# Kernel optimization log

Measured on AMD Instinct MI355X. Metric: run time of the kernel, lower is better.

The kernel has to match this reference:

```python
import jax, jax.numpy as jnp
import numpy as np

NODES_PER_GRAPH = 1430  # hard-coded stride in the original forward
GENE0 = 1421            # first gene node index per graph
N_HEADS = 9


def gcn_conv(x, W, b, src, dst, n):
    """PyG-style GCNConv: D^-1/2 (A+I) D^-1/2 X W + b (self-loops added)."""
    h = x @ W  # [N, out]
    ones = jnp.ones(src.shape, jnp.float32)
    deg = jax.ops.segment_sum(ones, dst, num_segments=n) + 1.0  # +1 self-loop
    dinv = jax.lax.rsqrt(deg)
    norm = dinv[src] * dinv[dst]  # [E]
    agg = jax.ops.segment_sum(norm[:, None] * h[src], dst, num_segments=n)
    agg = agg + (dinv * dinv)[:, None] * h  # self-loop contribution
    return agg + b


def setup_inputs() -> dict:
    key = jax.random.key(0)
    ks = jax.random.split(key, 8)
    n_graphs = 512
    n = NODES_PER_GRAPH * n_graphs  # 732160 nodes
    e = n * 8                        # avg degree 8
    x = jax.random.normal(ks[0], (n, 1), jnp.float32)
    edge_index = jax.random.randint(ks[1], (2, e), 0, n, jnp.int32)
    y = jnp.zeros((n_graphs * N_HEADS,), jnp.int32)  # only y.size(0) is used
    W1 = jax.random.normal(ks[2], (1, 16), jnp.float32) * 0.5
    b1 = jnp.zeros((16,), jnp.float32)
    W2 = jax.random.normal(ks[3], (16, 16), jnp.float32) * 0.25
    b2 = jnp.zeros((16,), jnp.float32)
    fw1 = jax.random.normal(ks[4], (N_HEADS, 16, 8), jnp.float32) * 0.25
    fb1 = jnp.zeros((N_HEADS, 8), jnp.float32)
    fw2 = jax.random.normal(ks[5], (N_HEADS, 8, 1), jnp.float32) * 0.35
    fb2 = jnp.zeros((N_HEADS, 1), jnp.float32)
    return {"x": x, "edge_index": edge_index, "y": y, "W1": W1, "b1": b1,
            "W2": W2, "b2": b2, "fw1": fw1, "fb1": fb1, "fw2": fw2, "fb2": fb2}


def reference(x, edge_index, y, W1, b1, W2, b2, fw1, fb1, fw2, fb2):
    n = x.shape[0]
    src, dst = edge_index[0], edge_index[1]
    h = jax.nn.relu(gcn_conv(x, W1, b1, src, dst, n))
    # F.dropout(p=0.4) treated as identity (deterministic eval reference)
    h = jax.nn.relu(gcn_conv(h, W2, b2, src, dst, n))
    n_graphs = y.shape[0] // N_HEADS
    # fused version of the per-gene gather loop: idx[g, k] = 1421+g + k*1430
    idx = (GENE0 + jnp.arange(N_HEADS)[:, None]
           + jnp.arange(n_graphs)[None, :] * NODES_PER_GRAPH)  # [9, G]
    g = h[idx]  # [9, G, 16]
    z = jax.nn.relu(jnp.einsum('gnf,gfh->gnh', g, fw1) + fb1[:, None, :])
    pred = jnp.einsum('gnh,gho->gno', z, fw2) + fb2[:, None, :]  # [9, G, 1]
    return tuple(pred[i] for i in range(N_HEADS))
```

## Files before the change

### kernel.cpp

```cpp
#include <hip/hip_runtime.h>

#define NODES 1430
#define GENE0 1421
#define NHEADS 9
#define HBINS 131072
#define HWORDS (HBINS / 8)
#define BHIST 1024
#define GMAX 64
#define QCAP 1024

__device__ __forceinline__ float frelu(float v) { return v > 0.f ? v : 0.f; }

__global__ __launch_bounds__(BHIST, 4)
void k_hist(const int* __restrict__ esrc, const int* __restrict__ edst,
            unsigned int* __restrict__ copies,
            int* __restrict__ gene_cnt, int* __restrict__ gene_src,
            unsigned int* __restrict__ flagw,
            int e, int K, int R) {
    __shared__ unsigned int lds[HWORDS];
    int id = blockIdx.x;
    int k, r;
    if ((K & 7) == 0) {
        int xcd = id & 7;
        int slot = id >> 3;
        int cin = slot / R;
        k = xcd * (K >> 3) + cin;
        r = slot - cin * R;
    } else {
        k = id / R;
        r = id - k * R;
    }
    const int tid = threadIdx.x;
    {
        uint4* l4 = (uint4*)lds;
        for (int w = tid; w < HWORDS / 4; w += BHIST) l4[w] = make_uint4(0, 0, 0, 0);
    }
    __syncthreads();

    const unsigned int lo = (unsigned int)r * HBINS;
    const int e4 = e >> 2;
    const int Q = (e4 + K - 1) / K;
    const int beg = k * Q;
    const int end = min(beg + Q, e4);
    const int4* ed4 = (const int4*)edst;
    const int len = (end > beg) ? (end - beg) : 0;
    const int eighth = len >> 3;

    auto proc = [&](int4 d4) {
#pragma unroll
        for (int c = 0; c < 4; c++) {
            unsigned int d = (unsigned int)((&d4.x)[c]);
            unsigned int rel = d - lo;
            if (rel < HBINS)
                atomicAdd(&lds[rel >> 3], 1u << ((rel & 7u) * 4u));
        }
    };

    for (int i = tid; i < eighth; i += BHIST) {
        int j0 = beg + i;
        int4 v0 = ed4[j0];
        int4 v1 = ed4[j0 + eighth];
        int4 v2 = ed4[j0 + 2 * eighth];
        int4 v3 = ed4[j0 + 3 * eighth];
        int4 v4 = ed4[j0 + 4 * eighth];
        int4 v5 = ed4[j0 + 5 * eighth];
        int4 v6 = ed4[j0 + 6 * eighth];
        int4 v7 = ed4[j0 + 7 * eighth];
        proc(v0); proc(v1); proc(v2); proc(v3);
        proc(v4); proc(v5); proc(v6); proc(v7);
    }
    for (int i = (eighth << 3) + tid; i < len; i += BHIST) {
        proc(ed4[beg + i]);
    }

    {
        int sbeg = beg + (int)(((long long)len * r) / R);
        int send = beg + (int)(((long long)len * (r + 1)) / R);
        for (int j = sbeg + tid; j < send; j += BHIST) {
            int4 d4 = ed4[j];
#pragma unroll
            for (int c = 0; c < 4; c++) {
                unsigned int d = (unsigned int)((&d4.x)[c]);
                unsigned int graph = d / NODES;
                unsigned int pos = d - graph * NODES;
                if (pos >= GENE0) {
                    int s = esrc[4 * j + c];
                    atomicOr(&flagw[(unsigned)s >> 5], 1u << (s & 31));
                    int g = (int)(graph * NHEADS + (pos - GENE0));
                    int p = atomicAdd(gene_cnt + g, 1);
                    if (p < GMAX) gene_src[(g << 6) + p] = s;
                }
            }
        }
    }

    if (k == 0) {
        for (int j = (e4 << 2) + tid; j < e; j += BHIST) {
            unsigned int d = (unsigned int)edst[j];
            unsigned int rel = d - lo;
            if (rel < HBINS)
                atomicAdd(&lds[rel >> 3], 1u << ((rel & 7u) * 4u));
            if (r == 0) {
                unsigned int graph = d / NODES;
                unsigned int pos = d - graph * NODES;
                if (pos >= GENE0) {
                    int s = esrc[j];
                    atomicOr(&flagw[(unsigned)s >> 5], 1u << (s & 31));
                    int g = (int)(graph * NHEADS + (pos - GENE0));
                    int p = atomicAdd(gene_cnt + g, 1);
                    if (p < GMAX) gene_src[(g << 6) + p] = s;
                }
            }
        }
    }
    __syncthreads();
    uint4* dst4 = (uint4*)(copies + ((size_t)k * R + r) * HWORDS);
    const uint4* l4 = (const uint4*)lds;
    for (int w = tid; w < HWORDS / 4; w += BHIST) dst4[w] = l4[w];
}

__global__ void k_reduce(const unsigned int* __restrict__ copies,
                         const float* __restrict__ x,
                         float2* __restrict__ dx, float* __restrict__ t,
                         unsigned int* __restrict__ flagw,
                         int n, int K, int Wtot) {
    int w = blockIdx.x * blockDim.x + threadIdx.x;
    if (w >= Wtot) return;
    const unsigned int M = 0x0F0F0F0Fu;
    unsigned int ev[8] = {0, 0, 0, 0, 0, 0, 0, 0};
    unsigned int od[8] = {0, 0, 0, 0, 0, 0, 0, 0};
    int k = 0;
    for (; k + 8 <= K; k += 8) {
#pragma unroll
        for (int s = 0; s < 8; s++) {
            unsigned int u = copies[(size_t)(k + s) * Wtot + w];
            ev[s] += u & M; od[s] += (u >> 4) & M;
        }
    }
    for (; k < K; k++) {
        unsigned int u = copies[(size_t)k * Wtot + w];
        ev[0] += u & M; od[0] += (u >> 4) & M;
    }
    unsigned int evn = ((ev[0] + ev[1]) + (ev[2] + ev[3])) + ((ev[4] + ev[5]) + (ev[6] + ev[7]));
    unsigned int odd = ((od[0] + od[1]) + (od[2] + od[3])) + ((od[4] + od[5]) + (od[6] + od[7]));
    int i0 = w << 3;
    float v[8];
#pragma unroll
    for (int b = 0; b < 4; b++) {
        v[2 * b]     = (float)((evn >> (8 * b)) & 0xFFu);
        v[2 * b + 1] = (float)((odd >> (8 * b)) & 0xFFu);
    }
#pragma unroll
    for (int b = 0; b < 8; b++) v[b] = rsqrtf(v[b] + 1.f);
    float4 z4 = {0.f, 0.f, 0.f, 0.f};
    if (i0 + 7 < n) {
        float4 xa = *(const float4*)(x + i0);
        float4 xb = *(const float4*)(x + i0 + 4);
        float4 p0 = {v[0], v[0] * xa.x, v[1], v[1] * xa.y};
        float4 p1 = {v[2], v[2] * xa.z, v[3], v[3] * xa.w};
        float4 p2 = {v[4], v[4] * xb.x, v[5], v[5] * xb.y};
        float4 p3 = {v[6], v[6] * xb.z, v[7], v[7] * xb.w};
        float4* dst = (float4*)(dx + i0);
        dst[0] = p0; dst[1] = p1; dst[2] = p2; dst[3] = p3;
        *(float4*)(t + i0) = z4;
        *(float4*)(t + i0 + 4) = z4;
    } else {
        for (int b = 0; b < 8; b++)
            if (i0 + b < n) {
                float xv = x[i0 + b];
                dx[i0 + b] = make_float2(v[b], v[b] * xv);
                t[i0 + b] = 0.f;
            }
    }
#pragma unroll
    for (int b = 0; b < 8; b++) {
        int i = i0 + b;
        if (i < n) {
            unsigned int graph = (unsigned int)i / NODES;
            unsigned int pos = (unsigned int)i - graph * NODES;
            if (pos >= GENE0) atomicOr(&flagw[(unsigned)i >> 5], 1u << (i & 31));
        }
    }
}

__global__ __launch_bounds__(256, 8)
void k_l1_scatter(const int* __restrict__ esrc, const int* __restrict__ edst,
                  const float2* __restrict__ dx,
                  const unsigned int* __restrict__ flagw,
                  float* __restrict__ t, int e) {
    __shared__ int2 q[QCAP];
    __shared__ int qn;
    const int tid = threadIdx.x;
    if (tid == 0) qn = 0;
    __syncthreads();

    const int4* ed4 = (const int4*)edst;
    const int4* es4 = (const int4*)esrc;
    const int e4 = e >> 2;
    const int g0 = blockIdx.x * 512;
#pragma unroll
    for (int u = 0; u < 2; u++) {
        int gi = g0 + u * 256 + tid;
        if (gi < e4) {
            int4 dd = ed4[gi];
            int4 ss = es4[gi];
#pragma unroll
            for (int c = 0; c < 4; c++) {
                int d = (&dd.x)[c];
                if ((flagw[(unsigned)d >> 5] >> (d & 31)) & 1u) {
                    int p = atomicAdd(&qn, 1);
                    if (p < QCAP) q[p] = make_int2((&ss.x)[c], d);
                    else atomicAdd(t + d, dx[(&ss.x)[c]].y);
                }
            }
        }
    }
    if (blockIdx.x == 0) {
        for (int j = (e4 << 2) + tid; j < e; j += 256) {
            int d = edst[j];
            if ((flagw[(unsigned)d >> 5] >> (d & 31)) & 1u) {
                int s = esrc[j];
                atomicAdd(t + d, dx[s].y);
            }
        }
    }
    __syncthreads();
    int m = min(qn, QCAP);
    for (int i = tid; i < m; i += 256) {
        int2 sd = q[i];
        atomicAdd(t + sd.y, dx[sd.x].y);
    }
}

__global__ void k_gene_final(const int* __restrict__ gene_cnt, const int* __restrict__ gene_src,
                             const float* __restrict__ t, const float2* __restrict__ dx,
                             const float* __restrict__ W1, const float* __restrict__ b1,
                             const float* __restrict__ W2, const float* __restrict__ b2,
                             const float* __restrict__ fw1, const float* __restrict__ fb1,
                             const float* __restrict__ fw2, const float* __restrict__ fb2,
                             float* __restrict__ out, int NG, int G) {
    int wid = (blockIdx.x * blockDim.x + threadIdx.x) >> 6;
    int lane = threadIdx.x & 63;
    if (wid >= NG) return;
    int g = wid;
    int graph = g / NHEADS;
    int head = g - graph * NHEADS;
    int node = graph * NODES + GENE0 + head;
    const int c = lane & 15;
    const int slot = lane >> 4;

    int cnt = min(gene_cnt[g], GMAX);

    float w1r[16], b1r[16], w2c[16];
#pragma unroll
    for (int kk = 0; kk < 16; kk++) {
        w1r[kk] = W1[kk];
        b1r[kk] = b1[kk];
        w2c[kk] = W2[kk * 16 + c];
    }
    float2 dn2 = dx[node];
    float tn = t[node];

    float acc = 0.f;
    const int base = g << 6;
    for (int i = slot; i < cnt; i += 8) {
        int s0 = gene_src[base + i];
        int i1 = i + 4;
        int s1 = (i1 < cnt) ? gene_src[base + i1] : -1;
        float2 a2 = dx[s0];
        float ta = t[s0];
        float2 b2v = (s1 >= 0) ? dx[s1] : make_float2(0.f, 0.f);
        float tb = (s1 >= 0) ? t[s1] : 0.f;
        {
            float us = a2.x * ta + a2.x * a2.y;
            float m = 0.f;
#pragma unroll
            for (int kk = 0; kk < 16; kk++)
                m += frelu(us * w1r[kk] + b1r[kk]) * w2c[kk];
            acc += a2.x * m;
        }
        if (s1 >= 0) {
            float us = b2v.x * tb + b2v.x * b2v.y;
            float m = 0.f;
#pragma unroll
            for (int kk = 0; kk < 16; kk++)
                m += frelu(us * w1r[kk] + b1r[kk]) * w2c[kk];
            acc += b2v.x * m;
        }
    }
    acc += __shfl_xor(acc, 16, 64);
    acc += __shfl_xor(acc, 32, 64);

    float dn = dn2.x;
    float un = dn * tn + dn * dn2.y;
    float h2 = 0.f;
#pragma unroll
    for (int kk = 0; kk < 16; kk++)
        h2 += frelu(un * w1r[kk] + b1r[kk]) * w2c[kk];
    float h = frelu(dn * acc + dn * dn * h2 + b2[c]);

    float hv[16];
#pragma unroll
    for (int c2 = 0; c2 < 16; c2++) hv[c2] = __shfl(h, c2, 64);

    int kk = lane & 7;
    float z = fb1[head * 8 + kk];
#pragma unroll
    for (int c2 = 0; c2 < 16; c2++) z += hv[c2] * fw1[head * 128 + c2 * 8 + kk];
    float term = frelu(z) * fw2[head * 8 + kk];
    term += __shfl_xor(term, 1, 64);
    term += __shfl_xor(term, 2, 64);
    term += __shfl_xor(term, 4, 64);
    if (lane == 0) out[head * G + graph] = fb2[head] + term;
}

extern "C" void kernel_launch(void* const* d_in, const int* in_sizes, int n_in,
                              void* d_out, int out_size, void* d_ws, size_t ws_size,
                              hipStream_t stream) {
    const float* x   = (const float*)d_in[0];
    const int*   ei  = (const int*)d_in[1];
    const float* W1  = (const float*)d_in[3];
    const float* b1  = (const float*)d_in[4];
    const float* W2  = (const float*)d_in[5];
    const float* b2  = (const float*)d_in[6];
    const float* fw1 = (const float*)d_in[7];
    const float* fb1 = (const float*)d_in[8];
    const float* fw2 = (const float*)d_in[9];
    const float* fb2 = (const float*)d_in[10];

    int n = in_sizes[0];
    int e = in_sizes[1] / 2;
    int G = in_sizes[2] / NHEADS;
    int NG = G * NHEADS;
    const int* esrc = ei;
    const int* edst = ei + e;

    char* ws = (char*)d_ws;
    size_t off = 0;
    auto alloc = [&](size_t bytes) {
        char* p = ws + off;
        off += (bytes + 255) & ~(size_t)255;
        return p;
    };
    int*   gene_cnt      = (int*)alloc((size_t)NG * 4);
    unsigned int* flagw  = (unsigned int*)alloc((size_t)((n + 31) / 32) * 4);
    size_t zero_bytes    = off;
    int*    gene_src     = (int*)alloc((size_t)NG * GMAX * 4);
    float*  t            = (float*)alloc((size_t)n * 4);
    float2* dx           = (float2*)alloc((size_t)n * 8);
    size_t fixed         = off;

    int R = (n + HBINS - 1) / HBINS;
    size_t per_copy = (size_t)R * HWORDS * 4;
    int K = 80;
    if (fixed + (size_t)K * per_copy > ws_size) {
        size_t avail = (ws_size > fixed) ? (ws_size - fixed) : 0;
        int kfit = (int)(avail / per_copy);
        if (kfit >= 8) kfit &= ~7;
        K = kfit < 1 ? 1 : (kfit < K ? kfit : K);
    }
    unsigned int* copies = (unsigned int*)alloc((size_t)K * per_copy);
    (void)n_in; (void)out_size;

    hipMemsetAsync(d_ws, 0, zero_bytes, stream);

    const int B = 256;
    k_hist<<<K * R, BHIST, 0, stream>>>(esrc, edst, copies, gene_cnt, gene_src,
                                        flagw, e, K, R);
    int Wtot = R * HWORDS;
    k_reduce<<<(Wtot + B - 1) / B, B, 0, stream>>>(copies, x, dx, t, flagw, n, K, Wtot);
    int nblk = ((e >> 2) + 511) / 512;
    k_l1_scatter<<<nblk, 256, 0, stream>>>(esrc, edst, dx, flagw, t, e);
    int waves_blocks = (NG * 64 + B - 1) / B;
    k_gene_final<<<waves_blocks, B, 0, stream>>>(gene_cnt, gene_src, t, dx,
                                                 W1, b1, W2, b2,
                                                 fw1, fb1, fw2, fb2,
                                                 (float*)d_out, NG, G);
}
```

Measured before the change: 167.2 us.

## Use dynamic 128KB LDS histogram to halve range passes over edges

The degree histogram moves to dynamic shared memory, and the kernel requests 128KB of LDS at runtime so each block covers 262144 nodes instead of 131072. This cuts the number of node ranges R from 6 to 3, so each edge chunk is read by half as many blocks. Histogram copy-out and reduce now skip words past n, which removes writes and reads for the padded tail. The trade-off is that the larger LDS footprint lowers occupancy per CU, and the path falls back to the old size if the attribute cannot be set.

```diff
diff --git a/kernel.cpp b/kernel.cpp
--- a/kernel.cpp
+++ b/kernel.cpp
@@ -3,8 +3,6 @@
 #define NODES 1430
 #define GENE0 1421
 #define NHEADS 9
-#define HBINS 131072
-#define HWORDS (HBINS / 8)
 #define BHIST 1024
 #define GMAX 64
 #define QCAP 1024
@@ -16,8 +14,8 @@
             unsigned int* __restrict__ copies,
             int* __restrict__ gene_cnt, int* __restrict__ gene_src,
             unsigned int* __restrict__ flagw,
-            int e, int K, int R) {
-    __shared__ unsigned int lds[HWORDS];
+            int e, int K, int R, int n, int hbins, int hwords) {
+    extern __shared__ unsigned int lds[];
     int id = blockIdx.x;
     int k, r;
     if ((K & 7) == 0) {
@@ -33,11 +31,13 @@
     const int tid = threadIdx.x;
     {
         uint4* l4 = (uint4*)lds;
-        for (int w = tid; w < HWORDS / 4; w += BHIST) l4[w] = make_uint4(0, 0, 0, 0);
+        const int hw4 = hwords >> 2;
+        for (int w = tid; w < hw4; w += BHIST) l4[w] = make_uint4(0, 0, 0, 0);
     }
     __syncthreads();
 
-    const unsigned int lo = (unsigned int)r * HBINS;
+    const unsigned int lo = (unsigned int)r * (unsigned int)hbins;
+    const unsigned int hb = (unsigned int)hbins;
     const int e4 = e >> 2;
     const int Q = (e4 + K - 1) / K;
     const int beg = k * Q;
@@ -51,7 +51,7 @@
         for (int c = 0; c < 4; c++) {
             unsigned int d = (unsigned int)((&d4.x)[c]);
             unsigned int rel = d - lo;
-            if (rel < HBINS)
+            if (rel < hb)
                 atomicAdd(&lds[rel >> 3], 1u << ((rel & 7u) * 4u));
         }
     };
@@ -98,7 +98,7 @@
         for (int j = (e4 << 2) + tid; j < e; j += BHIST) {
             unsigned int d = (unsigned int)edst[j];
             unsigned int rel = d - lo;
-            if (rel < HBINS)
+            if (rel < hb)
                 atomicAdd(&lds[rel >> 3], 1u << ((rel & 7u) * 4u));
             if (r == 0) {
                 unsigned int graph = d / NODES;
@@ -114,9 +114,12 @@
         }
     }
     __syncthreads();
-    uint4* dst4 = (uint4*)(copies + ((size_t)k * R + r) * HWORDS);
+    int wlimit = (n > (int)lo) ? ((n - (int)lo + 7) >> 3) : 0;
+    if (wlimit > hwords) wlimit = hwords;
+    int w4 = (wlimit + 3) >> 2;
+    uint4* dst4 = (uint4*)(copies + ((size_t)k * R + r) * hwords);
     const uint4* l4 = (const uint4*)lds;
-    for (int w = tid; w < HWORDS / 4; w += BHIST) dst4[w] = l4[w];
+    for (int w = tid; w < w4; w += BHIST) dst4[w] = l4[w];
 }
 
 __global__ void k_reduce(const unsigned int* __restrict__ copies,
@@ -126,6 +129,8 @@
                          int n, int K, int Wtot) {
     int w = blockIdx.x * blockDim.x + threadIdx.x;
     if (w >= Wtot) return;
+    int i0 = w << 3;
+    if (i0 >= n) return;
     const unsigned int M = 0x0F0F0F0Fu;
     unsigned int ev[8] = {0, 0, 0, 0, 0, 0, 0, 0};
     unsigned int od[8] = {0, 0, 0, 0, 0, 0, 0, 0};
@@ -143,7 +148,6 @@
     }
     unsigned int evn = ((ev[0] + ev[1]) + (ev[2] + ev[3])) + ((ev[4] + ev[5]) + (ev[6] + ev[7]));
     unsigned int odd = ((od[0] + od[1]) + (od[2] + od[3])) + ((od[4] + od[5]) + (od[6] + od[7]));
-    int i0 = w << 3;
     float v[8];
 #pragma unroll
     for (int b = 0; b < 4; b++) {
@@ -335,6 +339,16 @@
     const int* esrc = ei;
     const int* edst = ei + e;
 
+    static int HB_RT = 0;
+    if (HB_RT == 0) {
+        hipError_t st = hipFuncSetAttribute(
+            reinterpret_cast<const void*>(k_hist),
+            hipFuncAttributeMaxDynamicSharedMemorySize, 131072);
+        HB_RT = (st == hipSuccess) ? 262144 : 131072;
+    }
+    const int HB = HB_RT;
+    const int HW = HB >> 3;
+
     char* ws = (char*)d_ws;
     size_t off = 0;
     auto alloc = [&](size_t bytes) {
@@ -350,8 +364,8 @@
     float2* dx           = (float2*)alloc((size_t)n * 8);
     size_t fixed         = off;
 
-    int R = (n + HBINS - 1) / HBINS;
-    size_t per_copy = (size_t)R * HWORDS * 4;
+    int R = (n + HB - 1) / HB;
+    size_t per_copy = (size_t)R * HW * 4;
     int K = 80;
     if (fixed + (size_t)K * per_copy > ws_size) {
         size_t avail = (ws_size > fixed) ? (ws_size - fixed) : 0;
@@ -365,9 +379,10 @@
     hipMemsetAsync(d_ws, 0, zero_bytes, stream);
 
     const int B = 256;
-    k_hist<<<K * R, BHIST, 0, stream>>>(esrc, edst, copies, gene_cnt, gene_src,
-                                        flagw, e, K, R);
-    int Wtot = R * HWORDS;
+    size_t shmem = (size_t)HW * 4;
+    k_hist<<<K * R, BHIST, shmem, stream>>>(esrc, edst, copies, gene_cnt, gene_src,
+                                            flagw, e, K, R, n, HB, HW);
+    int Wtot = R * HW;
     k_reduce<<<(Wtot + B - 1) / B, B, 0, stream>>>(copies, x, dx, t, flagw, n, K, Wtot);
     int nblk = ((e >> 2) + 511) / 512;
     k_l1_scatter<<<nblk, 256, 0, stream>>>(esrc, edst, dx, flagw, t, e);
```

Result: no change. 168.8 us (+1.0%).

## Fuse all stages into one persistent kernel with software grid barriers

Applied to the files above, without the earlier changes.

Replaces the memset and four kernel launches with a single persistent kernel of 240 blocks that runs initialization, histogram, degree reduction, layer-1 scatter and gene head stages, separated by atomic grid barriers. The histogram uses larger 128KB LDS bins (3 ranges instead of 6). Gene-edge collection moves into the bin-owning block, and the flag bitmap is staged in LDS for the scatter filter. This removes launch gaps and memset overhead but relies on all blocks being co-resident, hard-codes the chunk counts and ignores the workspace size limit. It also runs the later stages on far fewer threads than the separate kernels did.

```diff
diff --git a/kernel.cpp b/kernel.cpp
--- a/kernel.cpp
+++ b/kernel.cpp
@@ -3,315 +3,356 @@
 #define NODES 1430
 #define GENE0 1421
 #define NHEADS 9
-#define HBINS 131072
+#define GMAX 64
+#define TPB 1024
+#define NB 240
+#define KCH 80
+#define RCH 3
+#define HBINS 262144
 #define HWORDS (HBINS / 8)
-#define BHIST 1024
-#define GMAX 64
-#define QCAP 1024
+#define QCAP2 4096
 
 __device__ __forceinline__ float frelu(float v) { return v > 0.f ? v : 0.f; }
 
-__global__ __launch_bounds__(BHIST, 4)
-void k_hist(const int* __restrict__ esrc, const int* __restrict__ edst,
-            unsigned int* __restrict__ copies,
-            int* __restrict__ gene_cnt, int* __restrict__ gene_src,
-            unsigned int* __restrict__ flagw,
-            int e, int K, int R) {
-    __shared__ unsigned int lds[HWORDS];
-    int id = blockIdx.x;
-    int k, r;
-    if ((K & 7) == 0) {
-        int xcd = id & 7;
-        int slot = id >> 3;
-        int cin = slot / R;
-        k = xcd * (K >> 3) + cin;
-        r = slot - cin * R;
-    } else {
-        k = id / R;
-        r = id - k * R;
-    }
+__device__ unsigned int g_cnt = 0;
+__device__ unsigned int g_gen = 0;
+
+__device__ __forceinline__ void grid_barrier() {
+    __syncthreads();
+    if (threadIdx.x == 0) {
+        __threadfence();
+        unsigned int old = __hip_atomic_load(&g_gen, __ATOMIC_ACQUIRE,
+                                             __HIP_MEMORY_SCOPE_AGENT);
+        unsigned int arr = __hip_atomic_fetch_add(&g_cnt, 1u, __ATOMIC_ACQ_REL,
+                                                  __HIP_MEMORY_SCOPE_AGENT) + 1u;
+        if (arr == gridDim.x) {
+            __hip_atomic_store(&g_cnt, 0u, __ATOMIC_RELAXED,
+                               __HIP_MEMORY_SCOPE_AGENT);
+            __hip_atomic_fetch_add(&g_gen, 1u, __ATOMIC_RELEASE,
+                                   __HIP_MEMORY_SCOPE_AGENT);
+        } else {
+            while (__hip_atomic_load(&g_gen, __ATOMIC_ACQUIRE,
+                                     __HIP_MEMORY_SCOPE_AGENT) == old) {
+                __builtin_amdgcn_s_sleep(1);
+            }
+        }
+    }
+    __syncthreads();
+}
+
+__global__ __launch_bounds__(TPB, 4)
+void k_fused(const int* __restrict__ esrc, const int* __restrict__ edst,
+             const float* __restrict__ x,
+             unsigned int* __restrict__ copies,
+             int* __restrict__ gene_cnt, int* __restrict__ gene_src,
+             unsigned int* __restrict__ flagw,
+             float* __restrict__ t, float2* __restrict__ dx,
+             const float* __restrict__ W1, const float* __restrict__ b1,
+             const float* __restrict__ W2, const float* __restrict__ b2,
+             const float* __restrict__ fw1, const float* __restrict__ fb1,
+             const float* __restrict__ fw2, const float* __restrict__ fb2,
+             float* __restrict__ out,
+             int n, int e, int G, int NG, int nw) {
+    extern __shared__ unsigned int lds[];
+    __shared__ int qn;
     const int tid = threadIdx.x;
+    const int bid = blockIdx.x;
+    const int gtid = bid * TPB + tid;
+    const int nthr = gridDim.x * TPB;
+
+    for (int i = gtid; i < NG; i += nthr) gene_cnt[i] = 0;
+    for (int w = gtid; w < nw; w += nthr) {
+        unsigned int m = 0;
+        int base = w << 5;
+#pragma unroll
+        for (int b = 0; b < 32; b++) {
+            int node = base + b;
+            if (node < n) {
+                unsigned int graph = (unsigned int)node / NODES;
+                unsigned int pos = (unsigned int)node - graph * NODES;
+                if (pos >= GENE0) m |= 1u << b;
+            }
+        }
+        flagw[w] = m;
+    }
+    grid_barrier();
+
     {
+        int xcd = bid & 7;
+        int slot = bid >> 3;
+        int cin = slot / RCH;
+        int k = xcd * (KCH >> 3) + cin;
+        int r = slot - cin * RCH;
+
         uint4* l4 = (uint4*)lds;
-        for (int w = tid; w < HWORDS / 4; w += BHIST) l4[w] = make_uint4(0, 0, 0, 0);
-    }
-    __syncthreads();
-
-    const unsigned int lo = (unsigned int)r * HBINS;
-    const int e4 = e >> 2;
-    const int Q = (e4 + K - 1) / K;
-    const int beg = k * Q;
-    const int end = min(beg + Q, e4);
-    const int4* ed4 = (const int4*)edst;
-    const int len = (end > beg) ? (end - beg) : 0;
-    const int eighth = len >> 3;
-
-    auto proc = [&](int4 d4) {
-#pragma unroll
-        for (int c = 0; c < 4; c++) {
-            unsigned int d = (unsigned int)((&d4.x)[c]);
-            unsigned int rel = d - lo;
-            if (rel < HBINS)
-                atomicAdd(&lds[rel >> 3], 1u << ((rel & 7u) * 4u));
-        }
-    };
-
-    for (int i = tid; i < eighth; i += BHIST) {
-        int j0 = beg + i;
-        int4 v0 = ed4[j0];
-        int4 v1 = ed4[j0 + eighth];
-        int4 v2 = ed4[j0 + 2 * eighth];
-        int4 v3 = ed4[j0 + 3 * eighth];
-        int4 v4 = ed4[j0 + 4 * eighth];
-        int4 v5 = ed4[j0 + 5 * eighth];
-        int4 v6 = ed4[j0 + 6 * eighth];
-        int4 v7 = ed4[j0 + 7 * eighth];
-        proc(v0); proc(v1); proc(v2); proc(v3);
-        proc(v4); proc(v5); proc(v6); proc(v7);
-    }
-    for (int i = (eighth << 3) + tid; i < len; i += BHIST) {
-        proc(ed4[beg + i]);
-    }
-
-    {
-        int sbeg = beg + (int)(((long long)len * r) / R);
-        int send = beg + (int)(((long long)len * (r + 1)) / R);
-        for (int j = sbeg + tid; j < send; j += BHIST) {
-            int4 d4 = ed4[j];
+        for (int w = tid; w < HWORDS / 4; w += TPB) l4[w] = make_uint4(0, 0, 0, 0);
+        __syncthreads();
+
+        const unsigned int lo = (unsigned int)r * HBINS;
+        const int e4 = e >> 2;
+        const int Q = (e4 + KCH - 1) / KCH;
+        const int beg = k * Q;
+        const int end = min(beg + Q, e4);
+        const int4* ed4 = (const int4*)edst;
+        const int len = (end > beg) ? (end - beg) : 0;
+        const int eighth = len >> 3;
+
+        auto proc = [&](int4 d4, int j4) {
 #pragma unroll
             for (int c = 0; c < 4; c++) {
                 unsigned int d = (unsigned int)((&d4.x)[c]);
-                unsigned int graph = d / NODES;
-                unsigned int pos = d - graph * NODES;
-                if (pos >= GENE0) {
-                    int s = esrc[4 * j + c];
-                    atomicOr(&flagw[(unsigned)s >> 5], 1u << (s & 31));
-                    int g = (int)(graph * NHEADS + (pos - GENE0));
-                    int p = atomicAdd(gene_cnt + g, 1);
-                    if (p < GMAX) gene_src[(g << 6) + p] = s;
-                }
-            }
-        }
-    }
-
-    if (k == 0) {
-        for (int j = (e4 << 2) + tid; j < e; j += BHIST) {
-            unsigned int d = (unsigned int)edst[j];
-            unsigned int rel = d - lo;
-            if (rel < HBINS)
-                atomicAdd(&lds[rel >> 3], 1u << ((rel & 7u) * 4u));
-            if (r == 0) {
-                unsigned int graph = d / NODES;
-                unsigned int pos = d - graph * NODES;
-                if (pos >= GENE0) {
-                    int s = esrc[j];
-                    atomicOr(&flagw[(unsigned)s >> 5], 1u << (s & 31));
-                    int g = (int)(graph * NHEADS + (pos - GENE0));
-                    int p = atomicAdd(gene_cnt + g, 1);
-                    if (p < GMAX) gene_src[(g << 6) + p] = s;
-                }
-            }
-        }
-    }
-    __syncthreads();
-    uint4* dst4 = (uint4*)(copies + ((size_t)k * R + r) * HWORDS);
-    const uint4* l4 = (const uint4*)lds;
-    for (int w = tid; w < HWORDS / 4; w += BHIST) dst4[w] = l4[w];
-}
-
-__global__ void k_reduce(const unsigned int* __restrict__ copies,
-                         const float* __restrict__ x,
-                         float2* __restrict__ dx, float* __restrict__ t,
-                         unsigned int* __restrict__ flagw,
-                         int n, int K, int Wtot) {
-    int w = blockIdx.x * blockDim.x + threadIdx.x;
-    if (w >= Wtot) return;
-    const unsigned int M = 0x0F0F0F0Fu;
-    unsigned int ev[8] = {0, 0, 0, 0, 0, 0, 0, 0};
-    unsigned int od[8] = {0, 0, 0, 0, 0, 0, 0, 0};
-    int k = 0;
-    for (; k + 8 <= K; k += 8) {
-#pragma unroll
-        for (int s = 0; s < 8; s++) {
-            unsigned int u = copies[(size_t)(k + s) * Wtot + w];
-            ev[s] += u & M; od[s] += (u >> 4) & M;
-        }
-    }
-    for (; k < K; k++) {
-        unsigned int u = copies[(size_t)k * Wtot + w];
-        ev[0] += u & M; od[0] += (u >> 4) & M;
-    }
-    unsigned int evn = ((ev[0] + ev[1]) + (ev[2] + ev[3])) + ((ev[4] + ev[5]) + (ev[6] + ev[7]));
-    unsigned int odd = ((od[0] + od[1]) + (od[2] + od[3])) + ((od[4] + od[5]) + (od[6] + od[7]));
-    int i0 = w << 3;
-    float v[8];
-#pragma unroll
-    for (int b = 0; b < 4; b++) {
-        v[2 * b]     = (float)((evn >> (8 * b)) & 0xFFu);
-        v[2 * b + 1] = (float)((odd >> (8 * b)) & 0xFFu);
-    }
-#pragma unroll
-    for (int b = 0; b < 8; b++) v[b] = rsqrtf(v[b] + 1.f);
-    float4 z4 = {0.f, 0.f, 0.f, 0.f};
-    if (i0 + 7 < n) {
-        float4 xa = *(const float4*)(x + i0);
-        float4 xb = *(const float4*)(x + i0 + 4);
-        float4 p0 = {v[0], v[0] * xa.x, v[1], v[1] * xa.y};
-        float4 p1 = {v[2], v[2] * xa.z, v[3], v[3] * xa.w};
-        float4 p2 = {v[4], v[4] * xb.x, v[5], v[5] * xb.y};
-        float4 p3 = {v[6], v[6] * xb.z, v[7], v[7] * xb.w};
-        float4* dst = (float4*)(dx + i0);
-        dst[0] = p0; dst[1] = p1; dst[2] = p2; dst[3] = p3;
-        *(float4*)(t + i0) = z4;
-        *(float4*)(t + i0 + 4) = z4;
-    } else {
-        for (int b = 0; b < 8; b++)
-            if (i0 + b < n) {
-                float xv = x[i0 + b];
-                dx[i0 + b] = make_float2(v[b], v[b] * xv);
-                t[i0 + b] = 0.f;
-            }
-    }
-#pragma unroll
-    for (int b = 0; b < 8; b++) {
-        int i = i0 + b;
-        if (i < n) {
-            unsigned int graph = (unsigned int)i / NODES;
-            unsigned int pos = (unsigned int)i - graph * NODES;
-            if (pos >= GENE0) atomicOr(&flagw[(unsigned)i >> 5], 1u << (i & 31));
-        }
-    }
-}
-
-__global__ __launch_bounds__(256, 8)
-void k_l1_scatter(const int* __restrict__ esrc, const int* __restrict__ edst,
-                  const float2* __restrict__ dx,
-                  const unsigned int* __restrict__ flagw,
-                  float* __restrict__ t, int e) {
-    __shared__ int2 q[QCAP];
-    __shared__ int qn;
-    const int tid = threadIdx.x;
-    if (tid == 0) qn = 0;
-    __syncthreads();
-
-    const int4* ed4 = (const int4*)edst;
-    const int4* es4 = (const int4*)esrc;
-    const int e4 = e >> 2;
-    const int g0 = blockIdx.x * 512;
-#pragma unroll
-    for (int u = 0; u < 2; u++) {
-        int gi = g0 + u * 256 + tid;
-        if (gi < e4) {
-            int4 dd = ed4[gi];
-            int4 ss = es4[gi];
+                unsigned int rel = d - lo;
+                if (rel < HBINS) {
+                    atomicAdd(&lds[rel >> 3], 1u << ((rel & 7u) * 4u));
+                    unsigned int graph = d / NODES;
+                    unsigned int pos = d - graph * NODES;
+                    if (pos >= GENE0) {
+                        int s = esrc[4 * j4 + c];
+                        atomicOr(&flagw[(unsigned)s >> 5], 1u << (s & 31));
+                        int g = (int)(graph * NHEADS + (pos - GENE0));
+                        int p = atomicAdd(gene_cnt + g, 1);
+                        if (p < GMAX) gene_src[(g << 6) + p] = s;
+                    }
+                }
+            }
+        };
+
+        for (int i = tid; i < eighth; i += TPB) {
+            int j0 = beg + i;
+            int4 v0 = ed4[j0];
+            int4 v1 = ed4[j0 + eighth];
+            int4 v2 = ed4[j0 + 2 * eighth];
+            int4 v3 = ed4[j0 + 3 * eighth];
+            int4 v4 = ed4[j0 + 4 * eighth];
+            int4 v5 = ed4[j0 + 5 * eighth];
+            int4 v6 = ed4[j0 + 6 * eighth];
+            int4 v7 = ed4[j0 + 7 * eighth];
+            proc(v0, j0);
+            proc(v1, j0 + eighth);
+            proc(v2, j0 + 2 * eighth);
+            proc(v3, j0 + 3 * eighth);
+            proc(v4, j0 + 4 * eighth);
+            proc(v5, j0 + 5 * eighth);
+            proc(v6, j0 + 6 * eighth);
+            proc(v7, j0 + 7 * eighth);
+        }
+        for (int i = (eighth << 3) + tid; i < len; i += TPB) {
+            proc(ed4[beg + i], beg + i);
+        }
+        if (k == 0) {
+            for (int j = (e4 << 2) + tid; j < e; j += TPB) {
+                unsigned int d = (unsigned int)edst[j];
+                unsigned int rel = d - lo;
+                if (rel < HBINS) {
+                    atomicAdd(&lds[rel >> 3], 1u << ((rel & 7u) * 4u));
+                    unsigned int graph = d / NODES;
+                    unsigned int pos = d - graph * NODES;
+                    if (pos >= GENE0) {
+                        int s = esrc[j];
+                        atomicOr(&flagw[(unsigned)s >> 5], 1u << (s & 31));
+                        int g = (int)(graph * NHEADS + (pos - GENE0));
+                        int p = atomicAdd(gene_cnt + g, 1);
+                        if (p < GMAX) gene_src[(g << 6) + p] = s;
+                    }
+                }
+            }
+        }
+        __syncthreads();
+        int wlimit = (n > (int)lo) ? ((n - (int)lo + 7) >> 3) : 0;
+        if (wlimit > HWORDS) wlimit = HWORDS;
+        int w4 = (wlimit + 3) >> 2;
+        uint4* dst4 = (uint4*)(copies + ((size_t)k * RCH + r) * HWORDS);
+        const uint4* s4 = (const uint4*)lds;
+        for (int w = tid; w < w4; w += TPB) dst4[w] = s4[w];
+    }
+    grid_barrier();
+
+    {
+        const int Wtot = RCH * HWORDS;
+        const unsigned int M = 0x0F0F0F0Fu;
+        for (int w = gtid; w < Wtot; w += nthr) {
+            int i0 = w << 3;
+            if (i0 >= n) continue;
+            unsigned int ev[8] = {0, 0, 0, 0, 0, 0, 0, 0};
+            unsigned int od[8] = {0, 0, 0, 0, 0, 0, 0, 0};
+            for (int k = 0; k + 8 <= KCH; k += 8) {
+#pragma unroll
+                for (int s = 0; s < 8; s++) {
+                    unsigned int u = copies[(size_t)(k + s) * Wtot + w];
+                    ev[s] += u & M; od[s] += (u >> 4) & M;
+                }
+            }
+            unsigned int evn = ((ev[0] + ev[1]) + (ev[2] + ev[3])) + ((ev[4] + ev[5]) + (ev[6] + ev[7]));
+            unsigned int odd = ((od[0] + od[1]) + (od[2] + od[3])) + ((od[4] + od[5]) + (od[6] + od[7]));
+            float v[8];
+#pragma unroll
+            for (int b = 0; b < 4; b++) {
+                v[2 * b]     = (float)((evn >> (8 * b)) & 0xFFu);
+                v[2 * b + 1] = (float)((odd >> (8 * b)) & 0xFFu);
+            }
+#pragma unroll
+            for (int b = 0; b < 8; b++) v[b] = rsqrtf(v[b] + 1.f);
+            float4 z4 = {0.f, 0.f, 0.f, 0.f};
+            if (i0 + 7 < n) {
+                float4 xa = *(const float4*)(x + i0);
+                float4 xb = *(const float4*)(x + i0 + 4);
+                float4 p0 = {v[0], v[0] * xa.x, v[1], v[1] * xa.y};
+                float4 p1 = {v[2], v[2] * xa.z, v[3], v[3] * xa.w};
+                float4 p2 = {v[4], v[4] * xb.x, v[5], v[5] * xb.y};
+                float4 p3 = {v[6], v[6] * xb.z, v[7], v[7] * xb.w};
+                float4* dst = (float4*)(dx + i0);
+                dst[0] = p0; dst[1] = p1; dst[2] = p2; dst[3] = p3;
+                *(float4*)(t + i0) = z4;
+                *(float4*)(t + i0 + 4) = z4;
+            } else {
+                for (int b = 0; b < 8; b++)
+                    if (i0 + b < n) {
+                        dx[i0 + b] = make_float2(v[b], v[b] * x[i0 + b]);
+                        t[i0 + b] = 0.f;
+                    }
+            }
+        }
+    }
+    grid_barrier();
+
+    {
+        unsigned int* fl = lds;
+        int2* q = (int2*)(lds + ((nw + 3) & ~3));
+        if (tid == 0) qn = 0;
+        const uint4* gl4 = (const uint4*)flagw;
+        uint4* fl4 = (uint4*)fl;
+        int nw4 = nw >> 2;
+        for (int w = tid; w < nw4; w += TPB) fl4[w] = gl4[w];
+        for (int w = (nw4 << 2) + tid; w < nw; w += TPB) fl[w] = flagw[w];
+        __syncthreads();
+
+        const int e4 = e >> 2;
+        const int Q = (e4 + gridDim.x - 1) / gridDim.x;
+        const int beg = bid * Q;
+        const int end = min(beg + Q, e4);
+        const int len = (end > beg) ? (end - beg) : 0;
+        const int4* ed4 = (const int4*)edst;
+
+        auto test = [&](int4 dd, int j4) {
 #pragma unroll
             for (int c = 0; c < 4; c++) {
                 int d = (&dd.x)[c];
-                if ((flagw[(unsigned)d >> 5] >> (d & 31)) & 1u) {
+                if ((fl[(unsigned)d >> 5] >> (d & 31)) & 1u) {
                     int p = atomicAdd(&qn, 1);
-                    if (p < QCAP) q[p] = make_int2((&ss.x)[c], d);
-                    else atomicAdd(t + d, dx[(&ss.x)[c]].y);
-                }
-            }
-        }
-    }
-    if (blockIdx.x == 0) {
-        for (int j = (e4 << 2) + tid; j < e; j += 256) {
-            int d = edst[j];
-            if ((flagw[(unsigned)d >> 5] >> (d & 31)) & 1u) {
-                int s = esrc[j];
-                atomicAdd(t + d, dx[s].y);
-            }
-        }
-    }
-    __syncthreads();
-    int m = min(qn, QCAP);
-    for (int i = tid; i < m; i += 256) {
-        int2 sd = q[i];
-        atomicAdd(t + sd.y, dx[sd.x].y);
-    }
-}
-
-__global__ void k_gene_final(const int* __restrict__ gene_cnt, const int* __restrict__ gene_src,
-                             const float* __restrict__ t, const float2* __restrict__ dx,
-                             const float* __restrict__ W1, const float* __restrict__ b1,
-                             const float* __restrict__ W2, const float* __restrict__ b2,
-                             const float* __restrict__ fw1, const float* __restrict__ fb1,
-                             const float* __restrict__ fw2, const float* __restrict__ fb2,
-                             float* __restrict__ out, int NG, int G) {
-    int wid = (blockIdx.x * blockDim.x + threadIdx.x) >> 6;
-    int lane = threadIdx.x & 63;
-    if (wid >= NG) return;
-    int g = wid;
-    int graph = g / NHEADS;
-    int head = g - graph * NHEADS;
-    int node = graph * NODES + GENE0 + head;
-    const int c = lane & 15;
-    const int slot = lane >> 4;
-
-    int cnt = min(gene_cnt[g], GMAX);
-
-    float w1r[16], b1r[16], w2c[16];
-#pragma unroll
-    for (int kk = 0; kk < 16; kk++) {
-        w1r[kk] = W1[kk];
-        b1r[kk] = b1[kk];
-        w2c[kk] = W2[kk * 16 + c];
-    }
-    float2 dn2 = dx[node];
-    float tn = t[node];
-
-    float acc = 0.f;
-    const int base = g << 6;
-    for (int i = slot; i < cnt; i += 8) {
-        int s0 = gene_src[base + i];
-        int i1 = i + 4;
-        int s1 = (i1 < cnt) ? gene_src[base + i1] : -1;
-        float2 a2 = dx[s0];
-        float ta = t[s0];
-        float2 b2v = (s1 >= 0) ? dx[s1] : make_float2(0.f, 0.f);
-        float tb = (s1 >= 0) ? t[s1] : 0.f;
-        {
-            float us = a2.x * ta + a2.x * a2.y;
-            float m = 0.f;
+                    if (p < QCAP2) q[p] = make_int2(4 * j4 + c, d);
+                    else atomicAdd(t + d, dx[esrc[4 * j4 + c]].y);
+                }
+            }
+        };
+
+        const int quarter = len >> 2;
+        for (int i = tid; i < quarter; i += TPB) {
+            int j0 = beg + i;
+            int4 d0 = ed4[j0];
+            int4 d1 = ed4[j0 + quarter];
+            int4 d2 = ed4[j0 + 2 * quarter];
+            int4 d3 = ed4[j0 + 3 * quarter];
+            test(d0, j0);
+            test(d1, j0 + quarter);
+            test(d2, j0 + 2 * quarter);
+            test(d3, j0 + 3 * quarter);
+        }
+        for (int i = (quarter << 2) + tid; i < len; i += TPB) {
+            test(ed4[beg + i], beg + i);
+        }
+        if (bid == 0) {
+            for (int j = (e4 << 2) + tid; j < e; j += TPB) {
+                int d = edst[j];
+                if ((fl[(unsigned)d >> 5] >> (d & 31)) & 1u)
+                    atomicAdd(t + d, dx[esrc[j]].y);
+            }
+        }
+        __syncthreads();
+        int m = min(qn, QCAP2);
+        for (int i = tid; i < m; i += TPB) q[i].x = esrc[q[i].x];
+        __syncthreads();
+        for (int i = tid; i < m; i += TPB) {
+            int2 sd = q[i];
+            atomicAdd(t + sd.y, dx[sd.x].y);
+        }
+    }
+    grid_barrier();
+
+    {
+        int wid = gtid >> 6;
+        int lane = tid & 63;
+        int nwaves = nthr >> 6;
+        const int c = lane & 15;
+        const int slot = lane >> 4;
+        for (int g = wid; g < NG; g += nwaves) {
+            int graph = g / NHEADS;
+            int head = g - graph * NHEADS;
+            int node = graph * NODES + GENE0 + head;
+            int cnt = min(gene_cnt[g], GMAX);
+
+            float w1r[16], b1r[16], w2c[16];
+#pragma unroll
+            for (int kk = 0; kk < 16; kk++) {
+                w1r[kk] = W1[kk];
+                b1r[kk] = b1[kk];
+                w2c[kk] = W2[kk * 16 + c];
+            }
+            float2 dn2 = dx[node];
+            float tn = t[node];
+
+            float acc = 0.f;
+            const int base = g << 6;
+            for (int i = slot; i < cnt; i += 8) {
+                int s0 = gene_src[base + i];
+                int i1 = i + 4;
+                int s1 = (i1 < cnt) ? gene_src[base + i1] : -1;
+                float2 a2 = dx[s0];
+                float ta = t[s0];
+                float2 b2v = (s1 >= 0) ? dx[s1] : make_float2(0.f, 0.f);
+                float tb = (s1 >= 0) ? t[s1] : 0.f;
+                {
+                    float us = a2.x * ta + a2.x * a2.y;
+                    float m2 = 0.f;
+#pragma unroll
+                    for (int kk = 0; kk < 16; kk++)
+                        m2 += frelu(us * w1r[kk] + b1r[kk]) * w2c[kk];
+                    acc += a2.x * m2;
+                }
+                if (s1 >= 0) {
+                    float us = b2v.x * tb + b2v.x * b2v.y;
+                    float m2 = 0.f;
+#pragma unroll
+                    for (int kk = 0; kk < 16; kk++)
+                        m2 += frelu(us * w1r[kk] + b1r[kk]) * w2c[kk];
+                    acc += b2v.x * m2;
+                }
+            }
+            acc += __shfl_xor(acc, 16, 64);
+            acc += __shfl_xor(acc, 32, 64);
+
+            float dn = dn2.x;
+            float un = dn * tn + dn * dn2.y;
+            float h2 = 0.f;
 #pragma unroll
             for (int kk = 0; kk < 16; kk++)
-                m += frelu(us * w1r[kk] + b1r[kk]) * w2c[kk];
-            acc += a2.x * m;
-        }
-        if (s1 >= 0) {
-            float us = b2v.x * tb + b2v.x * b2v.y;
-            float m = 0.f;
-#pragma unroll
-            for (int kk = 0; kk < 16; kk++)
-                m += frelu(us * w1r[kk] + b1r[kk]) * w2c[kk];
-            acc += b2v.x * m;
-        }
-    }
-    acc += __shfl_xor(acc, 16, 64);
-    acc += __shfl_xor(acc, 32, 64);
-
-    float dn = dn2.x;
-    float un = dn * tn + dn * dn2.y;
-    float h2 = 0.f;
-#pragma unroll
-    for (int kk = 0; kk < 16; kk++)
-        h2 += frelu(un * w1r[kk] + b1r[kk]) * w2c[kk];
-    float h = frelu(dn * acc + dn * dn * h2 + b2[c]);
-
-    float hv[16];
-#pragma unroll
-    for (int c2 = 0; c2 < 16; c2++) hv[c2] = __shfl(h, c2, 64);
-
-    int kk = lane & 7;
-    float z = fb1[head * 8 + kk];
-#pragma unroll
-    for (int c2 = 0; c2 < 16; c2++) z += hv[c2] * fw1[head * 128 + c2 * 8 + kk];
-    float term = frelu(z) * fw2[head * 8 + kk];
-    term += __shfl_xor(term, 1, 64);
-    term += __shfl_xor(term, 2, 64);
-    term += __shfl_xor(term, 4, 64);
-    if (lane == 0) out[head * G + graph] = fb2[head] + term;
+                h2 += frelu(un * w1r[kk] + b1r[kk]) * w2c[kk];
+            float h = frelu(dn * acc + dn * dn * h2 + b2[c]);
+
+            float hv[16];
+#pragma unroll
+            for (int c2 = 0; c2 < 16; c2++) hv[c2] = __shfl(h, c2, 64);
+
+            int kk = lane & 7;
+            float z = fb1[head * 8 + kk];
+#pragma unroll
+            for (int c2 = 0; c2 < 16; c2++) z += hv[c2] * fw1[head * 128 + c2 * 8 + kk];
+            float term = frelu(z) * fw2[head * 8 + kk];
+            term += __shfl_xor(term, 1, 64);
+            term += __shfl_xor(term, 2, 64);
+            term += __shfl_xor(term, 4, 64);
+            if (lane == 0) out[head * G + graph] = fb2[head] + term;
+        }
+    }
 }
 
 extern "C" void kernel_launch(void* const* d_in, const int* in_sizes, int n_in,
@@ -334,6 +375,14 @@
     int NG = G * NHEADS;
     const int* esrc = ei;
     const int* edst = ei + e;
+    int nw = (n + 31) / 32;
+
+    static int ATTR = 0;
+    if (!ATTR) {
+        hipFuncSetAttribute(reinterpret_cast<const void*>(k_fused),
+                            hipFuncAttributeMaxDynamicSharedMemorySize, 131072);
+        ATTR = 1;
+    }
 
     char* ws = (char*)d_ws;
     size_t off = 0;
@@ -342,38 +391,16 @@
         off += (bytes + 255) & ~(size_t)255;
         return p;
     };
-    int*   gene_cnt      = (int*)alloc((size_t)NG * 4);
-    unsigned int* flagw  = (unsigned int*)alloc((size_t)((n + 31) / 32) * 4);
-    size_t zero_bytes    = off;
-    int*    gene_src     = (int*)alloc((size_t)NG * GMAX * 4);
-    float*  t            = (float*)alloc((size_t)n * 4);
-    float2* dx           = (float2*)alloc((size_t)n * 8);
-    size_t fixed         = off;
-
-    int R = (n + HBINS - 1) / HBINS;
-    size_t per_copy = (size_t)R * HWORDS * 4;
-    int K = 80;
-    if (fixed + (size_t)K * per_copy > ws_size) {
-        size_t avail = (ws_size > fixed) ? (ws_size - fixed) : 0;
-        int kfit = (int)(avail / per_copy);
-        if (kfit >= 8) kfit &= ~7;
-        K = kfit < 1 ? 1 : (kfit < K ? kfit : K);
-    }
-    unsigned int* copies = (unsigned int*)alloc((size_t)K * per_copy);
-    (void)n_in; (void)out_size;
-
-    hipMemsetAsync(d_ws, 0, zero_bytes, stream);
-
-    const int B = 256;
-    k_hist<<<K * R, BHIST, 0, stream>>>(esrc, edst, copies, gene_cnt, gene_src,
-                                        flagw, e, K, R);
-    int Wtot = R * HWORDS;
-    k_reduce<<<(Wtot + B - 1) / B, B, 0, stream>>>(copies, x, dx, t, flagw, n, K, Wtot);
-    int nblk = ((e >> 2) + 511) / 512;
-    k_l1_scatter<<<nblk, 256, 0, stream>>>(esrc, edst, dx, flagw, t, e);
-    int waves_blocks = (NG * 64 + B - 1) / B;
-    k_gene_final<<<waves_blocks, B, 0, stream>>>(gene_cnt, gene_src, t, dx,
-                                                 W1, b1, W2, b2,
-                                                 fw1, fb1, fw2, fb2,
-                                                 (float*)d_out, NG, G);
+    int*    gene_cnt = (int*)alloc((size_t)NG * 4);
+    unsigned int* flagw = (unsigned int*)alloc((size_t)nw * 4);
+    int*    gene_src = (int*)alloc((size_t)NG * GMAX * 4);
+    float*  t        = (float*)alloc((size_t)n * 4);
+    float2* dx       = (float2*)alloc((size_t)n * 8);
+    unsigned int* copies = (unsigned int*)alloc((size_t)KCH * RCH * HWORDS * 4);
+    (void)n_in; (void)out_size; (void)ws_size;
+
+    k_fused<<<NB, TPB, 131072, stream>>>(esrc, edst, x, copies,
+                                         gene_cnt, gene_src, flagw, t, dx,
+                                         W1, b1, W2, b2, fw1, fb1, fw2, fb2,
+                                         (float*)d_out, n, e, G, NG, nw);
 }
```

Result: slower. 355.8 us (+112.8%).
